# Kernel optimization log

Hardware: AMD Instinct MI355X
Metric: run time of the kernel (lower is better)

The kernel has to match this reference:

```python
import jax, jax.numpy as jnp
import numpy as np


def _banded_diag_mean(a, b, r):
    """For each (batch i, row j) return mean of (a[i] @ b[i].T)[j, j-r:j+r+1],
    computed without materializing the LxL matrix. Windows are clipped to
    [max(0,j-r), min(L, j+r+1)].  a, b: [B, L, D]."""
    B, L, _ = a.shape
    sums = jnp.zeros((B, L), a.dtype)
    counts = jnp.zeros((L,), a.dtype)
    for d in range(-r, r + 1):  # small fixed set of 2r+1 diagonals
        if d >= 0:
            dots = jnp.einsum('bld,bld->bl', a[:, :L - d], b[:, d:])
            sums = sums.at[:, :L - d].add(dots)
            counts = counts.at[:L - d].add(1.0)
        else:
            dots = jnp.einsum('bld,bld->bl', a[:, -d:], b[:, :L + d])
            sums = sums.at[:, -d:].add(dots)
            counts = counts.at[-d:].add(1.0)
    return sums / counts


def setup_inputs() -> dict:
    key = jax.random.key(0)
    k1, k2, k3 = jax.random.split(key, 3)
    B, L, D_in, D_feat = 8, 1024, 512, 256
    return {
        'feature1': jax.random.normal(k1, (B, L, D_in), jnp.float32),
        'feature2': jax.random.normal(k2, (B, L, D_in), jnp.float32),
        'W': jax.random.normal(k3, (D_in, D_feat), jnp.float32) / np.sqrt(D_in),
        'b': jnp.zeros((D_feat,), jnp.float32),
        'positive_range_self': 4,
        'positive_range_tgt': 4,
    }


def reference(feature1, feature2, W, b, positive_range_self, positive_range_tgt):
    # MLPLayer projection (shared eval_func for both inputs): linear + relu
    emb_1 = jax.nn.relu(feature1 @ W + b)  # [B, L, Df]
    emb_2 = jax.nn.relu(feature2 @ W + b)  # [B, L, Df]
    B, L, Df = emb_1.shape
    N = B * L

    positive = jnp.einsum('bld,bld->bl', emb_1, emb_2)  # [B, L]
    if positive_range_self > 0:
        positive = positive + _banded_diag_mean(emb_1, emb_1, positive_range_self)
        positive = positive + _banded_diag_mean(emb_2, emb_2, positive_range_self)
    if positive_range_tgt > 0:
        positive = positive + _banded_diag_mean(emb_1, emb_2, positive_range_tgt)
    positive = positive.reshape(N)

    e1 = emb_1.reshape(N, Df)
    e2 = emb_2.reshape(N, Df)
    sim_matrix = e1 @ e2.T  # [N, N]
    negative = jax.nn.logsumexp(sim_matrix, axis=-1) - jnp.log(jnp.asarray(N, sim_matrix.dtype))

    nce_loss = jnp.mean(-positive + negative)
    return nce_loss
```

## Files before the change

### kernel.cpp

```cpp
#include <hip/hip_runtime.h>
#include <hip/hip_bf16.h>
#include <math.h>

#define DIN 512
#define DF 256
#define LSEQ 1024
#define NTOT 8192

typedef __attribute__((ext_vector_type(8))) short short8;
typedef __attribute__((ext_vector_type(4))) short short4v;
typedef __attribute__((ext_vector_type(4))) float f32x4;

__device__ __forceinline__ short f2bf(float x) {
  union { float f; unsigned u; } un; un.f = x;
  unsigned r = un.u + 0x7fffu + ((un.u >> 16) & 1u);
  return (short)(r >> 16);
}
__device__ __forceinline__ float bf2f(short s) {
  union { unsigned u; float f; } un; un.u = ((unsigned)(unsigned short)s) << 16;
  return un.f;
}

__global__ __launch_bounds__(256) void prep_w_kernel(const float* __restrict__ W,
                                                     short* __restrict__ Wt) {
  int idx = blockIdx.x * 256 + threadIdx.x;
  int c = idx >> 9;
  int k = idx & (DIN - 1);
  Wt[idx] = f2bf(W[(size_t)k * DF + c]);
}

#define PBM 64
#define PBK 32
#define PPAD 40

__global__ __launch_bounds__(256) void proj_kernel(const float* __restrict__ f1,
                                                   const float* __restrict__ f2,
                                                   const short* __restrict__ Wt,
                                                   const float* __restrict__ bias,
                                                   short* __restrict__ emb1,
                                                   short* __restrict__ emb2) {
  const float* feat = blockIdx.y ? f2 : f1;
  short* emb = blockIdx.y ? emb2 : emb1;
  __shared__ short ldsA[PBM * PPAD];
  __shared__ short ldsB[DF * PPAD];
  const int tid = threadIdx.x;
  const int lane = tid & 63, wv = tid >> 6;
  const int wrow = (wv & 1) * 32, wcol = (wv >> 1) * 128;
  const int l15 = lane & 15, lk = (lane >> 4) * 8;
  const int rowbase = blockIdx.x * PBM;

  f32x4 acc[2][8];
#pragma unroll
  for (int mi = 0; mi < 2; ++mi)
#pragma unroll
    for (int nf = 0; nf < 8; ++nf) acc[mi][nf] = f32x4{0.f, 0.f, 0.f, 0.f};

  for (int kb = 0; kb < DIN; kb += PBK) {
    __syncthreads();
#pragma unroll
    for (int i = 0; i < 2; ++i) {
      int flat = tid * 2 + i;
      int r = flat >> 3, kq = (flat & 7) * 4;
      f32x4 v = *(const f32x4*)(feat + (size_t)(rowbase + r) * DIN + kb + kq);
      short4v h;
      h[0] = f2bf(v[0]); h[1] = f2bf(v[1]); h[2] = f2bf(v[2]); h[3] = f2bf(v[3]);
      *(short4v*)(ldsA + r * PPAD + kq) = h;
    }
#pragma unroll
    for (int i = 0; i < 4; ++i) {
      int flat = tid * 4 + i;
      int c = flat >> 2, kq = (flat & 3) * 8;
      short8 v = *(const short8*)(Wt + (size_t)c * DIN + kb + kq);
      *(short8*)(ldsB + c * PPAD + kq) = v;
    }
    __syncthreads();
    short8 af[2], bf[8];
#pragma unroll
    for (int mi = 0; mi < 2; ++mi)
      af[mi] = *(const short8*)(ldsA + (wrow + mi * 16 + l15) * PPAD + lk);
#pragma unroll
    for (int nf = 0; nf < 8; ++nf)
      bf[nf] = *(const short8*)(ldsB + (wcol + nf * 16 + l15) * PPAD + lk);
#pragma unroll
    for (int mi = 0; mi < 2; ++mi)
#pragma unroll
      for (int nf = 0; nf < 8; ++nf)
        acc[mi][nf] = __builtin_amdgcn_mfma_f32_16x16x32_bf16(af[mi], bf[nf], acc[mi][nf], 0, 0, 0);
  }
  const int r4 = (lane >> 4) * 4;
#pragma unroll
  for (int mi = 0; mi < 2; ++mi) {
    int row0 = rowbase + wrow + mi * 16 + r4;
#pragma unroll
    for (int nf = 0; nf < 8; ++nf) {
      int col = wcol + nf * 16 + l15;
      float bb = bias[col];
#pragma unroll
      for (int r = 0; r < 4; ++r) {
        float v = acc[mi][nf][r] + bb;
        v = v > 0.f ? v : 0.f;
        emb[(size_t)(row0 + r) * DF + col] = f2bf(v);
      }
    }
  }
}

__global__ __launch_bounds__(64) void positive_kernel(const short* __restrict__ emb1,
                                                      const short* __restrict__ emb2,
                                                      const int* __restrict__ prs,
                                                      const int* __restrict__ prt,
                                                      float* __restrict__ pos) {
  const int row = blockIdx.x;
  const int b = row >> 10, j = row & (LSEQ - 1);
  const int lane = threadIdx.x;
  const int rs = prs[0], rt = prt[0];
  float a1[4], a2[4];
  {
    short4v v1 = *(const short4v*)(emb1 + (size_t)row * DF + lane * 4);
    short4v v2 = *(const short4v*)(emb2 + (size_t)row * DF + lane * 4);
#pragma unroll
    for (int i = 0; i < 4; ++i) { a1[i] = bf2f(v1[i]); a2[i] = bf2f(v2[i]); }
  }
  float dot12 = 0.f, p11 = 0.f, p22 = 0.f, p12 = 0.f;
#pragma unroll
  for (int i = 0; i < 4; ++i) dot12 += a1[i] * a2[i];
  int rmax = rs > rt ? rs : rt;
  for (int d = -rmax; d <= rmax; ++d) {
    int k = j + d;
    if (k < 0 || k >= LSEQ) continue;
    size_t koff = (size_t)(b * LSEQ + k) * DF + lane * 4;
    short4v w1 = *(const short4v*)(emb1 + koff);
    short4v w2 = *(const short4v*)(emb2 + koff);
    float d11 = 0.f, d22 = 0.f, d12 = 0.f;
#pragma unroll
    for (int i = 0; i < 4; ++i) {
      float e1k = bf2f(w1[i]), e2k = bf2f(w2[i]);
      d11 += a1[i] * e1k;
      d22 += a2[i] * e2k;
      d12 += a1[i] * e2k;
    }
    if (d >= -rs && d <= rs) { p11 += d11; p22 += d22; }
    if (d >= -rt && d <= rt) { p12 += d12; }
  }
#pragma unroll
  for (int m = 1; m < 64; m <<= 1) {
    dot12 += __shfl_xor(dot12, m);
    p11 += __shfl_xor(p11, m);
    p22 += __shfl_xor(p22, m);
    p12 += __shfl_xor(p12, m);
  }
  if (lane == 0) {
    float res = dot12;
    if (rs > 0) {
      int lo = j - rs < 0 ? 0 : j - rs;
      int hi = j + rs > LSEQ - 1 ? LSEQ - 1 : j + rs;
      res += (p11 + p22) / (float)(hi - lo + 1);
    }
    if (rt > 0) {
      int lo = j - rt < 0 ? 0 : j - rt;
      int hi = j + rt > LSEQ - 1 ? LSEQ - 1 : j + rt;
      res += p12 / (float)(hi - lo + 1);
    }
    pos[row] = res;
  }
}

#define NBM 128
#define NBN 64
#define NCHUNK 8
#define CHW (NTOT / NCHUNK)
#define NT (CHW / NBN)

__global__ __launch_bounds__(256) void negative_kernel(const short* __restrict__ e1,
                                                       const short* __restrict__ e2,
                                                       float* __restrict__ mpart,
                                                       float* __restrict__ spart) {
  __shared__ short ldsB[NBN * DF];
  const int tid = threadIdx.x;
  const int lane = tid & 63, wv = tid >> 6;
  const int l15 = lane & 15, lk16 = lane >> 4;
  const int rb = blockIdx.x, chunk = blockIdx.y;
  const int rowbase = rb * NBM + wv * 32;
  const int colbase0 = chunk * CHW;

  short8 a[2][8];
#pragma unroll
  for (int mi = 0; mi < 2; ++mi)
#pragma unroll
    for (int ks = 0; ks < 8; ++ks)
      a[mi][ks] = *(const short8*)(e1 + (size_t)(rowbase + mi * 16 + l15) * DF + ks * 32 + lk16 * 8);

  float mrun[8], srun[8];
#pragma unroll
  for (int i = 0; i < 8; ++i) { mrun[i] = -1e30f; srun[i] = 0.f; }

  short8 st[8];
  {
    const short* src = e2 + (size_t)colbase0 * DF;
#pragma unroll
    for (int it = 0; it < 8; ++it) {
      int S = it * 256 + tid;
      int c = S >> 5, kblk = S & 31;
      st[it] = *(const short8*)(src + (size_t)c * DF + kblk * 8);
    }
  }
  for (int t = 0; t < NT; ++t) {
    __syncthreads();
#pragma unroll
    for (int it = 0; it < 8; ++it) {
      int S = it * 256 + tid;
      int c = S >> 5, kblk = S & 31;
      int slot = kblk ^ (c & 7);
      *(short8*)(ldsB + (c * 32 + slot) * 8) = st[it];
    }
    __syncthreads();
    if (t + 1 < NT) {
      const short* src = e2 + (size_t)(colbase0 + (t + 1) * NBN) * DF;
#pragma unroll
      for (int it = 0; it < 8; ++it) {
        int S = it * 256 + tid;
        int c = S >> 5, kblk = S & 31;
        st[it] = *(const short8*)(src + (size_t)c * DF + kblk * 8);
      }
    }
    f32x4 acc[2][4];
#pragma unroll
    for (int mi = 0; mi < 2; ++mi)
#pragma unroll
      for (int nf = 0; nf < 4; ++nf) acc[mi][nf] = f32x4{0.f, 0.f, 0.f, 0.f};
#pragma unroll
    for (int ks = 0; ks < 8; ++ks) {
      short8 bfr[4];
#pragma unroll
      for (int nf = 0; nf < 4; ++nf) {
        int c = nf * 16 + l15;
        int kblk = ks * 4 + lk16;
        int slot = kblk ^ (c & 7);
        bfr[nf] = *(const short8*)(ldsB + (c * 32 + slot) * 8);
      }
#pragma unroll
      for (int mi = 0; mi < 2; ++mi)
#pragma unroll
        for (int nf = 0; nf < 4; ++nf)
          acc[mi][nf] = __builtin_amdgcn_mfma_f32_16x16x32_bf16(a[mi][ks], bfr[nf], acc[mi][nf], 0, 0, 0);
    }
#pragma unroll
    for (int mi = 0; mi < 2; ++mi)
#pragma unroll
      for (int r = 0; r < 4; ++r) {
        int s8 = mi * 4 + r;
        float v0 = acc[mi][0][r], v1 = acc[mi][1][r], v2 = acc[mi][2][r], v3 = acc[mi][3][r];
        float mx = fmaxf(fmaxf(v0, v1), fmaxf(v2, v3));
        float mn = fmaxf(mrun[s8], mx);
        float sc = __expf(mrun[s8] - mn);
        float sm = __expf(v0 - mn) + __expf(v1 - mn) + __expf(v2 - mn) + __expf(v3 - mn);
        srun[s8] = srun[s8] * sc + sm;
        mrun[s8] = mn;
      }
  }
#pragma unroll
  for (int mi = 0; mi < 2; ++mi)
#pragma unroll
    for (int r = 0; r < 4; ++r) {
      int s8 = mi * 4 + r;
      float m = mrun[s8], s = srun[s8];
#pragma unroll
      for (int msk = 1; msk < 16; msk <<= 1) {
        float mo = __shfl_xor(m, msk);
        float so = __shfl_xor(s, msk);
        float mn = fmaxf(m, mo);
        s = s * __expf(m - mn) + so * __expf(mo - mn);
        m = mn;
      }
      if (l15 == 0) {
        int row = rowbase + mi * 16 + lk16 * 4 + r;
        mpart[chunk * NTOT + row] = m;
        spart[chunk * NTOT + row] = s;
      }
    }
}

__global__ __launch_bounds__(256) void finalize_kernel(const float* __restrict__ pos,
                                                       const float* __restrict__ mpart,
                                                       const float* __restrict__ spart,
                                                       float* __restrict__ out) {
  __shared__ float red[256];
  int tid = threadIdx.x;
  float acc = 0.f;
  for (int row = tid; row < NTOT; row += 256) {
    float m = -1e30f;
#pragma unroll
    for (int c = 0; c < NCHUNK; ++c) m = fmaxf(m, mpart[c * NTOT + row]);
    float s = 0.f;
#pragma unroll
    for (int c = 0; c < NCHUNK; ++c) s += spart[c * NTOT + row] * __expf(mpart[c * NTOT + row] - m);
    float lse = m + logf(s);
    acc += (lse - pos[row]);
  }
  red[tid] = acc;
  __syncthreads();
  for (int s = 128; s > 0; s >>= 1) {
    if (tid < s) red[tid] += red[tid + s];
    __syncthreads();
  }
  if (tid == 0) out[0] = red[0] / (float)NTOT - logf((float)NTOT);
}

extern "C" void kernel_launch(void* const* d_in, const int* in_sizes, int n_in,
                              void* d_out, int out_size, void* d_ws, size_t ws_size,
                              hipStream_t stream) {
  const float* f1 = (const float*)d_in[0];
  const float* f2 = (const float*)d_in[1];
  const float* W = (const float*)d_in[2];
  const float* bias = (const float*)d_in[3];
  const int* prs = (const int*)d_in[4];
  const int* prt = (const int*)d_in[5];
  float* out = (float*)d_out;

  char* ws = (char*)d_ws;
  short* Wt = (short*)(ws);
  short* emb1 = (short*)(ws + (256 << 10));
  short* emb2 = (short*)(ws + (256 << 10) + (4 << 20));
  float* pos = (float*)(ws + (256 << 10) + (8 << 20));
  float* mpart = (float*)(ws + (256 << 10) + (8 << 20) + (32 << 10));
  float* spart = (float*)(ws + (256 << 10) + (8 << 20) + (32 << 10) + (256 << 10));

  prep_w_kernel<<<(DF * DIN) / 256, 256, 0, stream>>>(W, Wt);
  proj_kernel<<<dim3(NTOT / PBM, 2), 256, 0, stream>>>(f1, f2, Wt, bias, emb1, emb2);
  positive_kernel<<<NTOT, 64, 0, stream>>>(emb1, emb2, prs, prt, pos);
  negative_kernel<<<dim3(NTOT / NBM, NCHUNK), 256, 0, stream>>>(emb1, emb2, mpart, spart);
  finalize_kernel<<<1, 256, 0, stream>>>(pos, mpart, spart, out);
}
```

Measured before the change: 103.7 us.

## Double-buffer negative GEMM with direct global-to-LDS loads, larger tiles, lazy rescale

The negative logsumexp kernel now loads e2 tiles straight into double-buffered LDS with global_load_lds and an XOR swizzle. This overlaps the next tile's fetch with the current MFMAs and drops the register staging. Each wave now computes 64 rows instead of 32 to raise reuse of the B tile, and column chunks double. The online softmax rescales only when the max grows by more than 8, cutting exp calls. The single-block finalize becomes a two-stage reduction. The cost is higher register and LDS pressure, which may limit occupancy.

New measurement: 112.4 us. +8.4%, slower.

```diff
diff --git a/kernel.cpp b/kernel.cpp
--- a/kernel.cpp
+++ b/kernel.cpp
@@ -19,6 +19,12 @@
 __device__ __forceinline__ float bf2f(short s) {
   union { unsigned u; float f; } un; un.u = ((unsigned)(unsigned short)s) << 16;
   return un.f;
+}
+
+typedef __attribute__((address_space(1))) const unsigned char AS1c;
+typedef __attribute__((address_space(3))) unsigned char AS3;
+__device__ __forceinline__ void gload16(const void* g, void* l) {
+  __builtin_amdgcn_global_load_lds((AS1c*)g, (AS3*)l, 16, 0, 0);
 }
 
 __global__ __launch_bounds__(256) void prep_w_kernel(const float* __restrict__ W,
@@ -165,67 +171,60 @@
   }
 }
 
-#define NBM 128
+#define NBM 256
 #define NBN 64
-#define NCHUNK 8
+#define NCHUNK 16
 #define CHW (NTOT / NCHUNK)
 #define NT (CHW / NBN)
 
-__global__ __launch_bounds__(256) void negative_kernel(const short* __restrict__ e1,
-                                                       const short* __restrict__ e2,
-                                                       float* __restrict__ mpart,
-                                                       float* __restrict__ spart) {
-  __shared__ short ldsB[NBN * DF];
+__global__ __launch_bounds__(256, 2) void negative_kernel(const short* __restrict__ e1,
+                                                          const short* __restrict__ e2,
+                                                          float* __restrict__ mpart,
+                                                          float* __restrict__ spart) {
+  __shared__ short ldsB[2][NBN * DF];
   const int tid = threadIdx.x;
   const int lane = tid & 63, wv = tid >> 6;
   const int l15 = lane & 15, lk16 = lane >> 4;
-  const int rb = blockIdx.x, chunk = blockIdx.y;
-  const int rowbase = rb * NBM + wv * 32;
-  const int colbase0 = chunk * CHW;
-
-  short8 a[2][8];
-#pragma unroll
-  for (int mi = 0; mi < 2; ++mi)
+  const int rowbase = blockIdx.x * NBM + wv * 64;
+  const int chunk = blockIdx.y;
+  const short* colbase = e2 + (size_t)(chunk * CHW) * DF;
+
+  short8 a[4][8];
+#pragma unroll
+  for (int mi = 0; mi < 4; ++mi)
 #pragma unroll
     for (int ks = 0; ks < 8; ++ks)
       a[mi][ks] = *(const short8*)(e1 + (size_t)(rowbase + mi * 16 + l15) * DF + ks * 32 + lk16 * 8);
 
-  float mrun[8], srun[8];
-#pragma unroll
-  for (int i = 0; i < 8; ++i) { mrun[i] = -1e30f; srun[i] = 0.f; }
-
-  short8 st[8];
-  {
-    const short* src = e2 + (size_t)colbase0 * DF;
-#pragma unroll
-    for (int it = 0; it < 8; ++it) {
-      int S = it * 256 + tid;
-      int c = S >> 5, kblk = S & 31;
-      st[it] = *(const short8*)(src + (size_t)c * DF + kblk * 8);
-    }
-  }
+  float mrun[16], srun[16];
+#pragma unroll
+  for (int i = 0; i < 16; ++i) { mrun[i] = -1e30f; srun[i] = 0.f; }
+
+#pragma unroll
+  for (int i = 0; i < 8; ++i) {
+    int L = i * 256 + tid;
+    int c = L >> 5, s = L & 31;
+    int kblk = s ^ (c & 31);
+    gload16(colbase + (size_t)c * DF + kblk * 8, (short*)ldsB[0] + (i * 256 + wv * 64) * 8);
+  }
+  __syncthreads();
+
   for (int t = 0; t < NT; ++t) {
-    __syncthreads();
-#pragma unroll
-    for (int it = 0; it < 8; ++it) {
-      int S = it * 256 + tid;
-      int c = S >> 5, kblk = S & 31;
-      int slot = kblk ^ (c & 7);
-      *(short8*)(ldsB + (c * 32 + slot) * 8) = st[it];
-    }
-    __syncthreads();
+    short* buf = (short*)ldsB[t & 1];
     if (t + 1 < NT) {
-      const short* src = e2 + (size_t)(colbase0 + (t + 1) * NBN) * DF;
-#pragma unroll
-      for (int it = 0; it < 8; ++it) {
-        int S = it * 256 + tid;
-        int c = S >> 5, kblk = S & 31;
-        st[it] = *(const short8*)(src + (size_t)c * DF + kblk * 8);
-      }
-    }
-    f32x4 acc[2][4];
-#pragma unroll
-    for (int mi = 0; mi < 2; ++mi)
+      const short* nb = colbase + (size_t)(t + 1) * NBN * DF;
+      short* dbuf = (short*)ldsB[(t + 1) & 1];
+#pragma unroll
+      for (int i = 0; i < 8; ++i) {
+        int L = i * 256 + tid;
+        int c = L >> 5, s = L & 31;
+        int kblk = s ^ (c & 31);
+        gload16(nb + (size_t)c * DF + kblk * 8, dbuf + (i * 256 + wv * 64) * 8);
+      }
+    }
+    f32x4 acc[4][4];
+#pragma unroll
+    for (int mi = 0; mi < 4; ++mi)
 #pragma unroll
       for (int nf = 0; nf < 4; ++nf) acc[mi][nf] = f32x4{0.f, 0.f, 0.f, 0.f};
 #pragma unroll
@@ -235,31 +234,34 @@
       for (int nf = 0; nf < 4; ++nf) {
         int c = nf * 16 + l15;
         int kblk = ks * 4 + lk16;
-        int slot = kblk ^ (c & 7);
-        bfr[nf] = *(const short8*)(ldsB + (c * 32 + slot) * 8);
-      }
-#pragma unroll
-      for (int mi = 0; mi < 2; ++mi)
+        int s = kblk ^ (c & 31);
+        bfr[nf] = *(const short8*)(buf + (c * 32 + s) * 8);
+      }
+#pragma unroll
+      for (int mi = 0; mi < 4; ++mi)
 #pragma unroll
         for (int nf = 0; nf < 4; ++nf)
           acc[mi][nf] = __builtin_amdgcn_mfma_f32_16x16x32_bf16(a[mi][ks], bfr[nf], acc[mi][nf], 0, 0, 0);
     }
 #pragma unroll
-    for (int mi = 0; mi < 2; ++mi)
+    for (int mi = 0; mi < 4; ++mi)
 #pragma unroll
       for (int r = 0; r < 4; ++r) {
         int s8 = mi * 4 + r;
         float v0 = acc[mi][0][r], v1 = acc[mi][1][r], v2 = acc[mi][2][r], v3 = acc[mi][3][r];
         float mx = fmaxf(fmaxf(v0, v1), fmaxf(v2, v3));
-        float mn = fmaxf(mrun[s8], mx);
-        float sc = __expf(mrun[s8] - mn);
-        float sm = __expf(v0 - mn) + __expf(v1 - mn) + __expf(v2 - mn) + __expf(v3 - mn);
-        srun[s8] = srun[s8] * sc + sm;
-        mrun[s8] = mn;
-      }
-  }
-#pragma unroll
-  for (int mi = 0; mi < 2; ++mi)
+        float mo = mrun[s8];
+        if (mx > mo + 8.f) {
+          srun[s8] *= __expf(mo - mx);
+          mo = mx;
+          mrun[s8] = mx;
+        }
+        srun[s8] += __expf(v0 - mo) + __expf(v1 - mo) + __expf(v2 - mo) + __expf(v3 - mo);
+      }
+    __syncthreads();
+  }
+#pragma unroll
+  for (int mi = 0; mi < 4; ++mi)
 #pragma unroll
     for (int r = 0; r < 4; ++r) {
       int s8 = mi * 4 + r;
@@ -280,30 +282,33 @@
     }
 }
 
-__global__ __launch_bounds__(256) void finalize_kernel(const float* __restrict__ pos,
-                                                       const float* __restrict__ mpart,
-                                                       const float* __restrict__ spart,
+__global__ __launch_bounds__(256) void finalize1_kernel(const float* __restrict__ pos,
+                                                        const float* __restrict__ mpart,
+                                                        const float* __restrict__ spart,
+                                                        float* __restrict__ partial) {
+  __shared__ float red[4];
+  int row = blockIdx.x * 256 + threadIdx.x;
+  float m = -1e30f;
+#pragma unroll
+  for (int c = 0; c < NCHUNK; ++c) m = fmaxf(m, mpart[c * NTOT + row]);
+  float s = 0.f;
+#pragma unroll
+  for (int c = 0; c < NCHUNK; ++c) s += spart[c * NTOT + row] * __expf(mpart[c * NTOT + row] - m);
+  float v = m + logf(s) - pos[row];
+#pragma unroll
+  for (int msk = 1; msk < 64; msk <<= 1) v += __shfl_xor(v, msk);
+  if ((threadIdx.x & 63) == 0) red[threadIdx.x >> 6] = v;
+  __syncthreads();
+  if (threadIdx.x == 0) partial[blockIdx.x] = red[0] + red[1] + red[2] + red[3];
+}
+
+__global__ __launch_bounds__(64) void finalize2_kernel(const float* __restrict__ partial,
                                                        float* __restrict__ out) {
-  __shared__ float red[256];
-  int tid = threadIdx.x;
-  float acc = 0.f;
-  for (int row = tid; row < NTOT; row += 256) {
-    float m = -1e30f;
-#pragma unroll
-    for (int c = 0; c < NCHUNK; ++c) m = fmaxf(m, mpart[c * NTOT + row]);
-    float s = 0.f;
-#pragma unroll
-    for (int c = 0; c < NCHUNK; ++c) s += spart[c * NTOT + row] * __expf(mpart[c * NTOT + row] - m);
-    float lse = m + logf(s);
-    acc += (lse - pos[row]);
-  }
-  red[tid] = acc;
-  __syncthreads();
-  for (int s = 128; s > 0; s >>= 1) {
-    if (tid < s) red[tid] += red[tid + s];
-    __syncthreads();
-  }
-  if (tid == 0) out[0] = red[0] / (float)NTOT - logf((float)NTOT);
+  int lane = threadIdx.x;
+  float v = lane < 32 ? partial[lane] : 0.f;
+#pragma unroll
+  for (int msk = 1; msk < 64; msk <<= 1) v += __shfl_xor(v, msk);
+  if (lane == 0) out[0] = v / (float)NTOT - logf((float)NTOT);
 }
 
 extern "C" void kernel_launch(void* const* d_in, const int* in_sizes, int n_in,
@@ -319,15 +324,17 @@
 
   char* ws = (char*)d_ws;
   short* Wt = (short*)(ws);
-  short* emb1 = (short*)(ws + (256 << 10));
-  short* emb2 = (short*)(ws + (256 << 10) + (4 << 20));
-  float* pos = (float*)(ws + (256 << 10) + (8 << 20));
-  float* mpart = (float*)(ws + (256 << 10) + (8 << 20) + (32 << 10));
-  float* spart = (float*)(ws + (256 << 10) + (8 << 20) + (32 << 10) + (256 << 10));
+  short* emb1 = (short*)(ws + 262144);
+  short* emb2 = (short*)(ws + 262144 + 4194304);
+  float* pos = (float*)(ws + 8650752);
+  float* mpart = (float*)(ws + 8683520);
+  float* spart = (float*)(ws + 9207808);
+  float* partial = (float*)(ws + 9732096);
 
   prep_w_kernel<<<(DF * DIN) / 256, 256, 0, stream>>>(W, Wt);
   proj_kernel<<<dim3(NTOT / PBM, 2), 256, 0, stream>>>(f1, f2, Wt, bias, emb1, emb2);
   positive_kernel<<<NTOT, 64, 0, stream>>>(emb1, emb2, prs, prt, pos);
   negative_kernel<<<dim3(NTOT / NBM, NCHUNK), 256, 0, stream>>>(emb1, emb2, mpart, spart);
-  finalize_kernel<<<1, 256, 0, stream>>>(pos, mpart, spart, out);
-}
+  finalize1_kernel<<<32, 256, 0, stream>>>(pos, mpart, spart, partial);
+  finalize2_kernel<<<1, 64, 0, stream>>>(partial, out);
+}
```
